# Kernel tuning notes

Measured on AMD Instinct MI355X. Metric: run time of the kernel, lower is better.

## Reference

```python
import jax, jax.numpy as jnp
import numpy as np

N_NODES = 50000
N_EDGES = 800000
IN_FEAT = 256
OUT_FEAT = 128
P_EDGE = 0.2   # edge dropout rate
P_NODE = 0.1   # node-feature dropout rate
BN_EPS = 1e-5


def setup_inputs() -> dict:
    key = jax.random.key(0)
    ks = jax.random.split(key, 8)
    features = jax.random.normal(ks[0], (N_NODES, IN_FEAT), dtype=jnp.float32)
    W = jax.random.normal(ks[1], (IN_FEAT, OUT_FEAT), dtype=jnp.float32) / np.sqrt(IN_FEAT)
    b = jnp.zeros((OUT_FEAT,), dtype=jnp.float32)
    gamma = jnp.ones((OUT_FEAT,), dtype=jnp.float32)
    beta = jnp.zeros((OUT_FEAT,), dtype=jnp.float32)
    src = jax.random.randint(ks[2], (N_EDGES,), 0, N_NODES, dtype=jnp.int64)
    dst = jax.random.randint(ks[3], (N_EDGES,), 0, N_NODES, dtype=jnp.int64)
    edge_rand = jax.random.uniform(ks[4], (N_EDGES,), dtype=jnp.float32)
    node_rand = jax.random.uniform(ks[5], (N_NODES, OUT_FEAT), dtype=jnp.float32)
    return {"features": features, "W": W, "b": b, "gamma": gamma, "beta": beta,
            "src": src, "dst": dst, "edge_rand": edge_rand, "node_rand": node_rand}


def reference(features, W, b, gamma, beta, src, dst, edge_rand, node_rand):
    dt = features.dtype
    # --- edge dropout: keep-mask over edges (no rescale, per DropEdge convention) ---
    emask = (edge_rand >= P_EDGE).astype(dt)                      # [E]
    # --- GCN conv, norm='both' on the dropped graph ---
    h = features @ W                                              # [N, out] (W first: out < in)
    deg_src = jax.ops.segment_sum(emask, src, num_segments=N_NODES)  # out-degrees
    deg_dst = jax.ops.segment_sum(emask, dst, num_segments=N_NODES)  # in-degrees
    coef = emask * jax.lax.rsqrt(jnp.maximum(deg_src[src], 1.0) * jnp.maximum(deg_dst[dst], 1.0))
    msg = h[src] * coef[:, None]                                  # [E, out]
    agg = jax.ops.segment_sum(msg, dst, num_segments=N_NODES) + b  # [N, out]
    # --- BatchNorm1d (training mode: batch statistics over nodes) ---
    mean = jnp.mean(agg, axis=0)
    var = jnp.var(agg, axis=0)
    y = (agg - mean) * jax.lax.rsqrt(var + BN_EPS) * gamma + beta
    # --- node-feature dropout (inverted scaling) ---
    nmask = (node_rand >= P_NODE).astype(dt) / (1.0 - P_NODE)
    return y * nmask
```

## Files before the change

### kernel.cpp

```cpp
#include <hip/hip_runtime.h>

#define N_NODES 50000
#define N_EDGES 800000
#define IN_FEAT 256
#define OUT_FEAT 128
#define P_EDGE 0.2f
#define P_NODE 0.1f
#define BN_EPS 1e-5f
#define NPART 8
#define CAP_Q 16
#define PART_STRIDE 800000
#define CAP 64
#define GEMM_BLOCKS 782
#define EDGE_BLOCKS 782
#define EG_BLOCKS 1568
#define ZERO_BLOCKS 782
#define PREPW_BLOCKS 128
#define MERGE_BLOCKS 196
#define AGG_BLOCKS 2048
#define FIN_BLOCKS 8

typedef __bf16 bf16x8 __attribute__((ext_vector_type(8)));
typedef float floatx4 __attribute__((ext_vector_type(4)));
typedef float f32x4 __attribute__((ext_vector_type(4)));
typedef int i32x4 __attribute__((ext_vector_type(4)));

__device__ inline float bflo(unsigned u) { return __uint_as_float(u << 16); }
__device__ inline float bfhi(unsigned u) { return __uint_as_float(u & 0xffff0000u); }

__global__ __launch_bounds__(256) void k_init(const float* __restrict__ W,
    uint4* __restrict__ zero_base, __bf16* __restrict__ Wt) {
  if (blockIdx.x < ZERO_BLOCKS) {
    int i = blockIdx.x * 256 + threadIdx.x;
    if (i < 200000) zero_base[i] = make_uint4(0u, 0u, 0u, 0u);
  } else {
    int idx = (blockIdx.x - ZERO_BLOCKS) * 256 + threadIdx.x;
    int k = idx >> 7, n = idx & 127;
    Wt[n * IN_FEAT + k] = (__bf16)W[idx];
  }
}

__device__ inline bf16x8 cvt8(f32x4 a, f32x4 b) {
  bf16x8 v;
  v[0] = (__bf16)a[0]; v[1] = (__bf16)a[1]; v[2] = (__bf16)a[2]; v[3] = (__bf16)a[3];
  v[4] = (__bf16)b[0]; v[5] = (__bf16)b[1]; v[6] = (__bf16)b[2]; v[7] = (__bf16)b[3];
  return v;
}

__device__ void edge_body(int ebid, int q,
    const int* __restrict__ src, const int* __restrict__ dst,
    const float* __restrict__ er, unsigned* __restrict__ deg_src_q,
    unsigned* __restrict__ deg_dst_q, unsigned short* __restrict__ parts) {
  unsigned* dsq = deg_src_q + q * N_NODES;
  unsigned* ddq = deg_dst_q + q * N_NODES;
  unsigned short* pq = parts + (size_t)q * PART_STRIDE;
  int t = ebid * 256 + threadIdx.x;
  if (t < N_EDGES / 4) {
    f32x4 e4 = ((const f32x4*)er)[t];
    i32x4 s4 = ((const i32x4*)src)[t];
    i32x4 d4 = ((const i32x4*)dst)[t];
    const bool k0 = e4[0] >= P_EDGE, k1 = e4[1] >= P_EDGE;
    const bool k2 = e4[2] >= P_EDGE, k3 = e4[3] >= P_EDGE;
    unsigned p0 = 0xffffffffu, p1 = 0xffffffffu, p2 = 0xffffffffu, p3 = 0xffffffffu;
    if (k0) p0 = atomicAdd(&ddq[d4[0]], 1u);
    if (k1) p1 = atomicAdd(&ddq[d4[1]], 1u);
    if (k2) p2 = atomicAdd(&ddq[d4[2]], 1u);
    if (k3) p3 = atomicAdd(&ddq[d4[3]], 1u);
    if (k0) atomicAdd(&dsq[s4[0]], 1u);
    if (k1) atomicAdd(&dsq[s4[1]], 1u);
    if (k2) atomicAdd(&dsq[s4[2]], 1u);
    if (k3) atomicAdd(&dsq[s4[3]], 1u);
    if (p0 < CAP_Q) pq[(unsigned)d4[0] * CAP_Q + p0] = (unsigned short)s4[0];
    if (p1 < CAP_Q) pq[(unsigned)d4[1] * CAP_Q + p1] = (unsigned short)s4[1];
    if (p2 < CAP_Q) pq[(unsigned)d4[2] * CAP_Q + p2] = (unsigned short)s4[2];
    if (p3 < CAP_Q) pq[(unsigned)d4[3] * CAP_Q + p3] = (unsigned short)s4[3];
  }
}

__device__ void gemm_body(int bid, const float* __restrict__ feat,
    const __bf16* __restrict__ Wt, __bf16* __restrict__ h) {
  __shared__ char lds[65536];
  const int t = threadIdx.x;

  const uint4* wsrc = (const uint4*)Wt;
#pragma unroll
  for (int i = 0; i < 16; i++) {
    int c = i * 256 + t;
    unsigned o = (unsigned)c * 16u;
    unsigned row = o >> 9;
    *(uint4*)(lds + (o ^ ((row & 7u) << 4))) = wsrc[c];
  }
  __syncthreads();

  const int lane = t & 63;
  const int wave = t >> 6;
  const int l16 = lane & 15;
  const int quad = lane >> 4;
  const int m0 = bid * 64 + wave * 16;

  int mload = m0 + l16;
  if (mload >= N_NODES) mload = N_NODES - 1;

  bf16x8 a[8];
#pragma unroll
  for (int kk = 0; kk < 8; kk++) {
    const f32x4* p = (const f32x4*)(feat + (size_t)mload * IN_FEAT + kk * 32 + quad * 8);
    a[kk] = cvt8(p[0], p[1]);
  }

  floatx4 acc[8];
#pragma unroll
  for (int g = 0; g < 8; g++) {
    const unsigned row = (unsigned)(g * 16 + l16);
    const unsigned base = row * 512u + (unsigned)quad * 16u;
    const unsigned swz = (row & 7u) << 4;
    floatx4 c = {0.f, 0.f, 0.f, 0.f};
#pragma unroll
    for (int kk = 0; kk < 8; kk++) {
      bf16x8 b = *(const bf16x8*)(lds + ((base + (unsigned)kk * 64u) ^ swz));
      c = __builtin_amdgcn_mfma_f32_16x16x32_bf16(a[kk], b, c, 0, 0, 0);
    }
    acc[g] = c;
  }
  __syncthreads();

  char* hb = lds + wave * 16384;
#pragma unroll
  for (int g = 0; g < 8; g++) {
#pragma unroll
    for (int r = 0; r < 4; r++) {
      unsigned row = (unsigned)(quad * 4 + r);
      unsigned o = row * 256u + (unsigned)(g * 16 + l16) * 2u;
      *(__bf16*)(hb + (o ^ ((row & 7u) << 4))) = (__bf16)acc[g][r];
    }
  }
#pragma unroll
  for (int j = 0; j < 4; j++) {
    unsigned row = (unsigned)(lane >> 4) + (unsigned)j * 4u;
    unsigned o = row * 256u + (unsigned)(lane & 15) * 16u;
    uint4 v = *(const uint4*)(hb + (o ^ ((row & 7u) << 4)));
    int grow = m0 + (int)row;
    if (grow < N_NODES)
      *(uint4*)((char*)h + (size_t)grow * 256 + (size_t)(lane & 15) * 16) = v;
  }
}

__global__ __launch_bounds__(256) void k_eg(const float* __restrict__ feat,
    const __bf16* __restrict__ Wt, __bf16* __restrict__ h,
    const int* __restrict__ src, const int* __restrict__ dst,
    const float* __restrict__ er, unsigned* __restrict__ deg_src_q,
    unsigned* __restrict__ deg_dst_q, unsigned short* __restrict__ parts) {
  const int bid = blockIdx.x;
  const int grp = bid >> 3;
  const int l8 = bid & 7;
  const int id = (grp >> 1) * 8 + l8;
  if ((grp & 1) == 0) {
    if (id < EDGE_BLOCKS) edge_body(id, l8, src, dst, er, deg_src_q, deg_dst_q, parts);
  } else {
    if (id < GEMM_BLOCKS) gemm_body(id, feat, Wt, h);
  }
}

__global__ __launch_bounds__(256) void k_merge(const unsigned* __restrict__ deg_src_q,
    const unsigned* __restrict__ deg_dst_q, const unsigned short* __restrict__ parts,
    unsigned short* __restrict__ bucket, unsigned short* __restrict__ ct,
    unsigned char* __restrict__ deg_src_m) {
  int n = blockIdx.x * 256 + threadIdx.x;
  if (n >= N_NODES) return;
  unsigned ts = 0;
#pragma unroll
  for (int q = 0; q < NPART; q++) ts += deg_src_q[q * N_NODES + n];
  deg_src_m[n] = (unsigned char)(ts > 255u ? 255u : ts);
  unsigned short* bo = bucket + (size_t)n * CAP;
  unsigned w = 0, tt = 0;
#pragma unroll
  for (int q = 0; q < NPART; q++) {
    unsigned c = deg_dst_q[q * N_NODES + n];
    tt += c;
    c = c > CAP_Q ? CAP_Q : c;
    const unsigned short* pq = parts + (size_t)q * PART_STRIDE + (unsigned)n * CAP_Q;
    for (unsigned i = 0; i < c; i++) {
      if (w < CAP) bo[w++] = pq[i];
    }
  }
  tt = tt > 255u ? 255u : tt;
  ct[n] = (unsigned short)(w | (tt << 8));
}

__global__ __launch_bounds__(256) void k_agg(const unsigned short* __restrict__ h,
    const unsigned short* __restrict__ bucket, const unsigned char* __restrict__ deg_src_m,
    const unsigned short* __restrict__ ct, const float* __restrict__ bias,
    float* __restrict__ out, float* __restrict__ psum, float* __restrict__ pssq) {
  const int wid = threadIdx.x >> 6;
  const int lane = threadIdx.x & 63;
  const int g = lane >> 4;
  const int cl = lane & 15;
  const int wave_global = blockIdx.x * 4 + wid;

  float b8[8];
#pragma unroll
  for (int j = 0; j < 8; j++) b8[j] = bias[cl * 8 + j];

  float s8[8], ss8[8];
#pragma unroll
  for (int j = 0; j < 8; j++) { s8[j] = 0.f; ss8[j] = 0.f; }

  for (int d = wave_global; d < N_NODES; d += AGG_BLOCKS * 4) {
    const unsigned c2 = ct[d];
    const unsigned lim = c2 & 0xffu;
    const unsigned tot = c2 >> 8;
    const unsigned base = (unsigned)d * CAP;
    float acc[8];
#pragma unroll
    for (int j = 0; j < 8; j++) acc[j] = 0.f;

#pragma unroll 2
    for (unsigned i = 0; i < lim; i += 4) {
      unsigned e = i + (unsigned)g;
      bool valid = e < lim;
      unsigned idx = (unsigned)bucket[base + (valid ? e : 0u)];
      unsigned dg = deg_src_m[idx];
      float r = valid ? rsqrtf((float)(dg ? dg : 1u)) : 0.f;
      uint4 u = *(const uint4*)(h + (size_t)idx * OUT_FEAT + cl * 8);
      acc[0] = fmaf(bflo(u.x), r, acc[0]);
      acc[1] = fmaf(bfhi(u.x), r, acc[1]);
      acc[2] = fmaf(bflo(u.y), r, acc[2]);
      acc[3] = fmaf(bfhi(u.y), r, acc[3]);
      acc[4] = fmaf(bflo(u.z), r, acc[4]);
      acc[5] = fmaf(bfhi(u.z), r, acc[5]);
      acc[6] = fmaf(bflo(u.w), r, acc[6]);
      acc[7] = fmaf(bfhi(u.w), r, acc[7]);
    }
#pragma unroll
    for (int j = 0; j < 8; j++) {
      acc[j] += __shfl_xor(acc[j], 16);
      acc[j] += __shfl_xor(acc[j], 32);
    }
    if (g == 0) {
      float sc = rsqrtf((float)(tot ? tot : 1u));
      float o[8];
#pragma unroll
      for (int j = 0; j < 8; j++) {
        o[j] = fmaf(acc[j], sc, b8[j]);
        s8[j] += o[j];
        ss8[j] = fmaf(o[j], o[j], ss8[j]);
      }
      float4 o0 = make_float4(o[0], o[1], o[2], o[3]);
      float4 o1 = make_float4(o[4], o[5], o[6], o[7]);
      *(float4*)(out + (size_t)d * OUT_FEAT + cl * 8) = o0;
      *(float4*)(out + (size_t)d * OUT_FEAT + cl * 8 + 4) = o1;
    }
  }

  __shared__ float ls[4][16][8], lss[4][16][8];
  if (g == 0) {
#pragma unroll
    for (int j = 0; j < 8; j++) { ls[wid][cl][j] = s8[j]; lss[wid][cl][j] = ss8[j]; }
  }
  __syncthreads();
  if (threadIdx.x < 128) {
    int pcl = threadIdx.x >> 3, pj = threadIdx.x & 7;
    float t = ls[0][pcl][pj] + ls[1][pcl][pj] + ls[2][pcl][pj] + ls[3][pcl][pj];
    float t2 = lss[0][pcl][pj] + lss[1][pcl][pj] + lss[2][pcl][pj] + lss[3][pcl][pj];
    psum[blockIdx.x * OUT_FEAT + threadIdx.x] = t;
    pssq[blockIdx.x * OUT_FEAT + threadIdx.x] = t2;
  }
}

__global__ __launch_bounds__(256) void k_fin(const float* __restrict__ psum,
    const float* __restrict__ pssq, const float* __restrict__ gamma,
    const float* __restrict__ beta, float* __restrict__ a_coef,
    float* __restrict__ b_coef) {
  const int col16 = threadIdx.x & 15;
  const int slice = threadIdx.x >> 4;
  const int c = blockIdx.x * 16 + col16;
  float t = 0.f, t2 = 0.f;
  for (int b = slice; b < AGG_BLOCKS; b += 16) {
    t += psum[b * OUT_FEAT + c];
    t2 += pssq[b * OUT_FEAT + c];
  }
  __shared__ float S[16][17], S2[16][17];
  S[slice][col16] = t;
  S2[slice][col16] = t2;
  __syncthreads();
  if (threadIdx.x < 16) {
    float ts = 0.f, tss = 0.f;
#pragma unroll
    for (int s = 0; s < 16; s++) { ts += S[s][threadIdx.x]; tss += S2[s][threadIdx.x]; }
    int cc = blockIdx.x * 16 + threadIdx.x;
    float mean = ts * (1.0f / N_NODES);
    float var = tss * (1.0f / N_NODES) - mean * mean;
    float a = gamma[cc] * rsqrtf(var + BN_EPS);
    a_coef[cc] = a;
    b_coef[cc] = fmaf(-mean, a, beta[cc]);
  }
}

__global__ __launch_bounds__(256) void k_norm(float* __restrict__ out,
    const float* __restrict__ node_rand, const float* __restrict__ a_coef,
    const float* __restrict__ b_coef) {
  const size_t total4 = (size_t)N_NODES * OUT_FEAT / 4;
  size_t i = (size_t)blockIdx.x * 256 + threadIdx.x;
  if (i < total4) {
    int c0 = (int)((i * 4) & 127);
    f32x4 v = ((const f32x4*)out)[i];
    f32x4 nr = ((const f32x4*)node_rand)[i];
    f32x4 a = *(const f32x4*)(a_coef + c0);
    f32x4 b = *(const f32x4*)(b_coef + c0);
    const float inv = 1.0f / (1.0f - P_NODE);
    f32x4 o;
    o[0] = (nr[0] >= P_NODE ? inv : 0.f) * fmaf(v[0], a[0], b[0]);
    o[1] = (nr[1] >= P_NODE ? inv : 0.f) * fmaf(v[1], a[1], b[1]);
    o[2] = (nr[2] >= P_NODE ? inv : 0.f) * fmaf(v[2], a[2], b[2]);
    o[3] = (nr[3] >= P_NODE ? inv : 0.f) * fmaf(v[3], a[3], b[3]);
    ((f32x4*)out)[i] = o;
  }
}

extern "C" void kernel_launch(void* const* d_in, const int* in_sizes, int n_in,
                              void* d_out, int out_size, void* d_ws, size_t ws_size,
                              hipStream_t stream) {
  const float* feat  = (const float*)d_in[0];
  const float* W     = (const float*)d_in[1];
  const float* bias  = (const float*)d_in[2];
  const float* gamma = (const float*)d_in[3];
  const float* beta  = (const float*)d_in[4];
  const int*   src   = (const int*)d_in[5];
  const int*   dst   = (const int*)d_in[6];
  const float* er    = (const float*)d_in[7];
  const float* nr    = (const float*)d_in[8];
  float* out = (float*)d_out;

  char* ws = (char*)d_ws;
  __bf16*         h         = (__bf16*)        (ws + 0);
  unsigned short* parts     = (unsigned short*)(ws + 12800000);
  float*          psum      = (float*)         (ws + 12800000);
  float*          pssq      = (float*)         (ws + 13848576);
  unsigned short* bucket    = (unsigned short*)(ws + 25600000);
  __bf16*         Wt        = (__bf16*)        (ws + 32000000);
  unsigned*       deg_src_q = (unsigned*)      (ws + 32065536);
  unsigned*       deg_dst_q = (unsigned*)      (ws + 33665536);
  unsigned short* ct        = (unsigned short*)(ws + 35265536);
  unsigned char*  deg_src_m = (unsigned char*) (ws + 35365632);
  float*          a_coef    = (float*)         (ws + 35415808);
  float*          b_coef    = (float*)         (ws + 35416320);

  k_init<<<ZERO_BLOCKS + PREPW_BLOCKS, 256, 0, stream>>>(
      W, (uint4*)(ws + 32065536), Wt);
  k_eg<<<EG_BLOCKS, 256, 0, stream>>>(feat, Wt, h, src, dst, er,
      deg_src_q, deg_dst_q, parts);
  k_merge<<<MERGE_BLOCKS, 256, 0, stream>>>(deg_src_q, deg_dst_q, parts,
      bucket, ct, deg_src_m);
  k_agg<<<AGG_BLOCKS, 256, 0, stream>>>((const unsigned short*)h, bucket,
      deg_src_m, ct, bias, out, psum, pssq);
  k_fin<<<FIN_BLOCKS, 256, 0, stream>>>(psum, pssq, gamma, beta, a_coef, b_coef);
  k_norm<<<(N_NODES * OUT_FEAT / 4 + 255) / 256, 256, 0, stream>>>(out, nr, a_coef, b_coef);
}
```

Baseline: 286.6 us.

## Drop merge and finalize kernels; read partitioned buckets directly in aggregation

Removes the k_merge pass by having the aggregation kernel read the eight per-partition edge buckets directly, using a per-node prefix over partition counts to locate each edge. The source-degree count becomes a single shared atomic array instead of eight partitions. The BatchNorm finalize kernel is folded into k_agg through atomic partial sums and a last-block-done counter. The GEMM now stages W in four 16KB K-chunks instead of one 64KB LDS tile, which should allow higher occupancy at the cost of extra barriers. Risks include more atomic contention on deg_src and extra index arithmetic in the inner gather loop.

```diff
diff --git a/kernel.cpp b/kernel.cpp
--- a/kernel.cpp
+++ b/kernel.cpp
@@ -10,15 +10,13 @@
 #define NPART 8
 #define CAP_Q 16
 #define PART_STRIDE 800000
-#define CAP 64
 #define GEMM_BLOCKS 782
 #define EDGE_BLOCKS 782
 #define EG_BLOCKS 1568
-#define ZERO_BLOCKS 782
+#define ZERO_BLOCKS 442
+#define ZERO_CHUNKS 113028
 #define PREPW_BLOCKS 128
-#define MERGE_BLOCKS 196
 #define AGG_BLOCKS 2048
-#define FIN_BLOCKS 8
 
 typedef __bf16 bf16x8 __attribute__((ext_vector_type(8)));
 typedef float floatx4 __attribute__((ext_vector_type(4)));
@@ -32,7 +30,7 @@
     uint4* __restrict__ zero_base, __bf16* __restrict__ Wt) {
   if (blockIdx.x < ZERO_BLOCKS) {
     int i = blockIdx.x * 256 + threadIdx.x;
-    if (i < 200000) zero_base[i] = make_uint4(0u, 0u, 0u, 0u);
+    if (i < ZERO_CHUNKS) zero_base[i] = make_uint4(0u, 0u, 0u, 0u);
   } else {
     int idx = (blockIdx.x - ZERO_BLOCKS) * 256 + threadIdx.x;
     int k = idx >> 7, n = idx & 127;
@@ -49,9 +47,8 @@
 
 __device__ void edge_body(int ebid, int q,
     const int* __restrict__ src, const int* __restrict__ dst,
-    const float* __restrict__ er, unsigned* __restrict__ deg_src_q,
+    const float* __restrict__ er, unsigned* __restrict__ deg_src,
     unsigned* __restrict__ deg_dst_q, unsigned short* __restrict__ parts) {
-  unsigned* dsq = deg_src_q + q * N_NODES;
   unsigned* ddq = deg_dst_q + q * N_NODES;
   unsigned short* pq = parts + (size_t)q * PART_STRIDE;
   int t = ebid * 256 + threadIdx.x;
@@ -66,10 +63,10 @@
     if (k1) p1 = atomicAdd(&ddq[d4[1]], 1u);
     if (k2) p2 = atomicAdd(&ddq[d4[2]], 1u);
     if (k3) p3 = atomicAdd(&ddq[d4[3]], 1u);
-    if (k0) atomicAdd(&dsq[s4[0]], 1u);
-    if (k1) atomicAdd(&dsq[s4[1]], 1u);
-    if (k2) atomicAdd(&dsq[s4[2]], 1u);
-    if (k3) atomicAdd(&dsq[s4[3]], 1u);
+    if (k0) atomicAdd(&deg_src[s4[0]], 1u);
+    if (k1) atomicAdd(&deg_src[s4[1]], 1u);
+    if (k2) atomicAdd(&deg_src[s4[2]], 1u);
+    if (k3) atomicAdd(&deg_src[s4[3]], 1u);
     if (p0 < CAP_Q) pq[(unsigned)d4[0] * CAP_Q + p0] = (unsigned short)s4[0];
     if (p1 < CAP_Q) pq[(unsigned)d4[1] * CAP_Q + p1] = (unsigned short)s4[1];
     if (p2 < CAP_Q) pq[(unsigned)d4[2] * CAP_Q + p2] = (unsigned short)s4[2];
@@ -79,19 +76,8 @@
 
 __device__ void gemm_body(int bid, const float* __restrict__ feat,
     const __bf16* __restrict__ Wt, __bf16* __restrict__ h) {
-  __shared__ char lds[65536];
+  __shared__ char lds[16384];
   const int t = threadIdx.x;
-
-  const uint4* wsrc = (const uint4*)Wt;
-#pragma unroll
-  for (int i = 0; i < 16; i++) {
-    int c = i * 256 + t;
-    unsigned o = (unsigned)c * 16u;
-    unsigned row = o >> 9;
-    *(uint4*)(lds + (o ^ ((row & 7u) << 4))) = wsrc[c];
-  }
-  __syncthreads();
-
   const int lane = t & 63;
   const int wave = t >> 6;
   const int l16 = lane & 15;
@@ -110,21 +96,33 @@
 
   floatx4 acc[8];
 #pragma unroll
-  for (int g = 0; g < 8; g++) {
-    const unsigned row = (unsigned)(g * 16 + l16);
-    const unsigned base = row * 512u + (unsigned)quad * 16u;
-    const unsigned swz = (row & 7u) << 4;
-    floatx4 c = {0.f, 0.f, 0.f, 0.f};
-#pragma unroll
-    for (int kk = 0; kk < 8; kk++) {
-      bf16x8 b = *(const bf16x8*)(lds + ((base + (unsigned)kk * 64u) ^ swz));
-      c = __builtin_amdgcn_mfma_f32_16x16x32_bf16(a[kk], b, c, 0, 0, 0);
-    }
-    acc[g] = c;
+  for (int g = 0; g < 8; g++) acc[g] = (floatx4){0.f, 0.f, 0.f, 0.f};
+
+#pragma unroll
+  for (int c = 0; c < 4; c++) {
+    __syncthreads();
+#pragma unroll
+    for (int i = 0; i < 4; i++) {
+      int ci = i * 256 + t;
+      int row = ci >> 3, kseg = ci & 7;
+      uint4 v = *(const uint4*)(Wt + (size_t)row * IN_FEAT + c * 64 + kseg * 8);
+      *(uint4*)(lds + ((unsigned)(row * 128 + kseg * 16) ^ ((unsigned)(row & 7) << 4))) = v;
+    }
+    __syncthreads();
+#pragma unroll
+    for (int g = 0; g < 8; g++) {
+      const unsigned row = (unsigned)(g * 16 + l16);
+      const unsigned swz = (row & 7u) << 4;
+#pragma unroll
+      for (int kk = 0; kk < 2; kk++) {
+        bf16x8 b = *(const bf16x8*)(lds + ((row * 128u + (unsigned)kk * 64u + (unsigned)quad * 16u) ^ swz));
+        acc[g] = __builtin_amdgcn_mfma_f32_16x16x32_bf16(a[c * 2 + kk], b, acc[g], 0, 0, 0);
+      }
+    }
   }
   __syncthreads();
 
-  char* hb = lds + wave * 16384;
+  char* hb = lds + wave * 4096;
 #pragma unroll
   for (int g = 0; g < 8; g++) {
 #pragma unroll
@@ -148,49 +146,25 @@
 __global__ __launch_bounds__(256) void k_eg(const float* __restrict__ feat,
     const __bf16* __restrict__ Wt, __bf16* __restrict__ h,
     const int* __restrict__ src, const int* __restrict__ dst,
-    const float* __restrict__ er, unsigned* __restrict__ deg_src_q,
+    const float* __restrict__ er, unsigned* __restrict__ deg_src,
     unsigned* __restrict__ deg_dst_q, unsigned short* __restrict__ parts) {
   const int bid = blockIdx.x;
   const int grp = bid >> 3;
   const int l8 = bid & 7;
   const int id = (grp >> 1) * 8 + l8;
   if ((grp & 1) == 0) {
-    if (id < EDGE_BLOCKS) edge_body(id, l8, src, dst, er, deg_src_q, deg_dst_q, parts);
+    if (id < EDGE_BLOCKS) edge_body(id, l8, src, dst, er, deg_src, deg_dst_q, parts);
   } else {
     if (id < GEMM_BLOCKS) gemm_body(id, feat, Wt, h);
   }
 }
 
-__global__ __launch_bounds__(256) void k_merge(const unsigned* __restrict__ deg_src_q,
-    const unsigned* __restrict__ deg_dst_q, const unsigned short* __restrict__ parts,
-    unsigned short* __restrict__ bucket, unsigned short* __restrict__ ct,
-    unsigned char* __restrict__ deg_src_m) {
-  int n = blockIdx.x * 256 + threadIdx.x;
-  if (n >= N_NODES) return;
-  unsigned ts = 0;
-#pragma unroll
-  for (int q = 0; q < NPART; q++) ts += deg_src_q[q * N_NODES + n];
-  deg_src_m[n] = (unsigned char)(ts > 255u ? 255u : ts);
-  unsigned short* bo = bucket + (size_t)n * CAP;
-  unsigned w = 0, tt = 0;
-#pragma unroll
-  for (int q = 0; q < NPART; q++) {
-    unsigned c = deg_dst_q[q * N_NODES + n];
-    tt += c;
-    c = c > CAP_Q ? CAP_Q : c;
-    const unsigned short* pq = parts + (size_t)q * PART_STRIDE + (unsigned)n * CAP_Q;
-    for (unsigned i = 0; i < c; i++) {
-      if (w < CAP) bo[w++] = pq[i];
-    }
-  }
-  tt = tt > 255u ? 255u : tt;
-  ct[n] = (unsigned short)(w | (tt << 8));
-}
-
 __global__ __launch_bounds__(256) void k_agg(const unsigned short* __restrict__ h,
-    const unsigned short* __restrict__ bucket, const unsigned char* __restrict__ deg_src_m,
-    const unsigned short* __restrict__ ct, const float* __restrict__ bias,
-    float* __restrict__ out, float* __restrict__ psum, float* __restrict__ pssq) {
+    const unsigned short* __restrict__ parts, const unsigned* __restrict__ deg_src,
+    const unsigned* __restrict__ deg_dst_q, const float* __restrict__ bias,
+    const float* __restrict__ gamma, const float* __restrict__ beta,
+    float* __restrict__ out, float* __restrict__ psum8, float* __restrict__ pssq8,
+    unsigned* __restrict__ done, float* __restrict__ a_coef, float* __restrict__ b_coef) {
   const int wid = threadIdx.x >> 6;
   const int lane = threadIdx.x & 63;
   const int g = lane >> 4;
@@ -206,10 +180,19 @@
   for (int j = 0; j < 8; j++) { s8[j] = 0.f; ss8[j] = 0.f; }
 
   for (int d = wave_global; d < N_NODES; d += AGG_BLOCKS * 4) {
-    const unsigned c2 = ct[d];
-    const unsigned lim = c2 & 0xffu;
-    const unsigned tot = c2 >> 8;
-    const unsigned base = (unsigned)d * CAP;
+    unsigned P[8];
+    unsigned run = 0, tot = 0;
+#pragma unroll
+    for (int q = 0; q < NPART; q++) {
+      unsigned c = deg_dst_q[q * N_NODES + d];
+      tot += c;
+      c = c > CAP_Q ? CAP_Q : c;
+      P[q] = run;
+      run += c;
+    }
+    const unsigned lim = run;
+    const unsigned dbase = (unsigned)d * CAP_Q;
+
     float acc[8];
 #pragma unroll
     for (int j = 0; j < 8; j++) acc[j] = 0.f;
@@ -218,8 +201,16 @@
     for (unsigned i = 0; i < lim; i += 4) {
       unsigned e = i + (unsigned)g;
       bool valid = e < lim;
-      unsigned idx = (unsigned)bucket[base + (valid ? e : 0u)];
-      unsigned dg = deg_src_m[idx];
+      unsigned ec = valid ? e : 0u;
+      unsigned qq = 0, off = 0;
+#pragma unroll
+      for (int j = 1; j < 8; j++) {
+        bool ge = ec >= P[j];
+        qq += ge ? 1u : 0u;
+        off = ge ? P[j] : off;
+      }
+      unsigned idx = (unsigned)parts[(size_t)qq * PART_STRIDE + dbase + (ec - off)];
+      unsigned dg = deg_src[idx];
       float r = valid ? rsqrtf((float)(dg ? dg : 1u)) : 0.f;
       uint4 u = *(const uint4*)(h + (size_t)idx * OUT_FEAT + cl * 8);
       acc[0] = fmaf(bflo(u.x), r, acc[0]);
@@ -258,41 +249,32 @@
     for (int j = 0; j < 8; j++) { ls[wid][cl][j] = s8[j]; lss[wid][cl][j] = ss8[j]; }
   }
   __syncthreads();
+  const int xs = (blockIdx.x & 7) * OUT_FEAT;
   if (threadIdx.x < 128) {
     int pcl = threadIdx.x >> 3, pj = threadIdx.x & 7;
-    float t = ls[0][pcl][pj] + ls[1][pcl][pj] + ls[2][pcl][pj] + ls[3][pcl][pj];
+    float tv = ls[0][pcl][pj] + ls[1][pcl][pj] + ls[2][pcl][pj] + ls[3][pcl][pj];
     float t2 = lss[0][pcl][pj] + lss[1][pcl][pj] + lss[2][pcl][pj] + lss[3][pcl][pj];
-    psum[blockIdx.x * OUT_FEAT + threadIdx.x] = t;
-    pssq[blockIdx.x * OUT_FEAT + threadIdx.x] = t2;
-  }
-}
-
-__global__ __launch_bounds__(256) void k_fin(const float* __restrict__ psum,
-    const float* __restrict__ pssq, const float* __restrict__ gamma,
-    const float* __restrict__ beta, float* __restrict__ a_coef,
-    float* __restrict__ b_coef) {
-  const int col16 = threadIdx.x & 15;
-  const int slice = threadIdx.x >> 4;
-  const int c = blockIdx.x * 16 + col16;
-  float t = 0.f, t2 = 0.f;
-  for (int b = slice; b < AGG_BLOCKS; b += 16) {
-    t += psum[b * OUT_FEAT + c];
-    t2 += pssq[b * OUT_FEAT + c];
-  }
-  __shared__ float S[16][17], S2[16][17];
-  S[slice][col16] = t;
-  S2[slice][col16] = t2;
+    atomicAdd(&psum8[xs + threadIdx.x], tv);
+    atomicAdd(&pssq8[xs + threadIdx.x], t2);
+  }
+  __threadfence();
   __syncthreads();
-  if (threadIdx.x < 16) {
+  __shared__ int lastf;
+  if (threadIdx.x == 0)
+    lastf = (atomicAdd(done, 1u) == (unsigned)(AGG_BLOCKS - 1));
+  __syncthreads();
+  if (lastf && threadIdx.x < 128) {
     float ts = 0.f, tss = 0.f;
 #pragma unroll
-    for (int s = 0; s < 16; s++) { ts += S[s][threadIdx.x]; tss += S2[s][threadIdx.x]; }
-    int cc = blockIdx.x * 16 + threadIdx.x;
+    for (int q = 0; q < NPART; q++) {
+      ts += atomicAdd(&psum8[q * OUT_FEAT + threadIdx.x], 0.f);
+      tss += atomicAdd(&pssq8[q * OUT_FEAT + threadIdx.x], 0.f);
+    }
     float mean = ts * (1.0f / N_NODES);
     float var = tss * (1.0f / N_NODES) - mean * mean;
-    float a = gamma[cc] * rsqrtf(var + BN_EPS);
-    a_coef[cc] = a;
-    b_coef[cc] = fmaf(-mean, a, beta[cc]);
+    float aa = gamma[threadIdx.x] * rsqrtf(var + BN_EPS);
+    a_coef[threadIdx.x] = aa;
+    b_coef[threadIdx.x] = fmaf(-mean, aa, beta[threadIdx.x]);
   }
 }
 
@@ -334,25 +316,20 @@
   char* ws = (char*)d_ws;
   __bf16*         h         = (__bf16*)        (ws + 0);
   unsigned short* parts     = (unsigned short*)(ws + 12800000);
-  float*          psum      = (float*)         (ws + 12800000);
-  float*          pssq      = (float*)         (ws + 13848576);
-  unsigned short* bucket    = (unsigned short*)(ws + 25600000);
-  __bf16*         Wt        = (__bf16*)        (ws + 32000000);
-  unsigned*       deg_src_q = (unsigned*)      (ws + 32065536);
-  unsigned*       deg_dst_q = (unsigned*)      (ws + 33665536);
-  unsigned short* ct        = (unsigned short*)(ws + 35265536);
-  unsigned char*  deg_src_m = (unsigned char*) (ws + 35365632);
-  float*          a_coef    = (float*)         (ws + 35415808);
-  float*          b_coef    = (float*)         (ws + 35416320);
+  __bf16*         Wt        = (__bf16*)        (ws + 25600000);
+  unsigned*       deg_src   = (unsigned*)      (ws + 25665536);
+  unsigned*       deg_dst_q = (unsigned*)      (ws + 25865536);
+  float*          psum8     = (float*)         (ws + 27465536);
+  float*          pssq8     = (float*)         (ws + 27469632);
+  unsigned*       done      = (unsigned*)      (ws + 27473728);
+  float*          a_coef    = (float*)         (ws + 27473984);
+  float*          b_coef    = (float*)         (ws + 27474496);
 
   k_init<<<ZERO_BLOCKS + PREPW_BLOCKS, 256, 0, stream>>>(
-      W, (uint4*)(ws + 32065536), Wt);
+      W, (uint4*)(ws + 25665536), Wt);
   k_eg<<<EG_BLOCKS, 256, 0, stream>>>(feat, Wt, h, src, dst, er,
-      deg_src_q, deg_dst_q, parts);
-  k_merge<<<MERGE_BLOCKS, 256, 0, stream>>>(deg_src_q, deg_dst_q, parts,
-      bucket, ct, deg_src_m);
-  k_agg<<<AGG_BLOCKS, 256, 0, stream>>>((const unsigned short*)h, bucket,
-      deg_src_m, ct, bias, out, psum, pssq);
-  k_fin<<<FIN_BLOCKS, 256, 0, stream>>>(psum, pssq, gamma, beta, a_coef, b_coef);
+      deg_src, deg_dst_q, parts);
+  k_agg<<<AGG_BLOCKS, 256, 0, stream>>>((const unsigned short*)h, parts,
+      deg_src, deg_dst_q, bias, gamma, beta, out, psum8, pssq8, done, a_coef, b_coef);
   k_norm<<<(N_NODES * OUT_FEAT / 4 + 255) / 256, 256, 0, stream>>>(out, nr, a_coef, b_coef);
 }
```

Result: slower. 445.2 us (+55.4%).
